# Performance work log

Measured on AMD Instinct MI355X. Metric: run time of the kernel, lower is better.

The kernel has to match this reference:

```python
import jax, jax.numpy as jnp
import numpy as np
import math

HIDDEN = 2048
N_HEADS = 16
N_KV_HEADS = 4
HEAD_DIM = HIDDEN // N_HEADS  # 128
MAX_POS = 4096
ROPE_THETA = 10000.0
B, S = 2, 2048


def _rope_tables():
    freqs = 1.0 / (ROPE_THETA ** (np.arange(0, HEAD_DIM, 2, dtype=np.float32) / HEAD_DIM))
    t = np.arange(MAX_POS, dtype=np.float32)
    f = np.outer(t, freqs)                      # [MAX_POS, HEAD_DIM/2]
    emb = np.concatenate([f, f], axis=-1)       # [MAX_POS, HEAD_DIM]
    return jnp.asarray(np.cos(emb)), jnp.asarray(np.sin(emb))


def setup_inputs() -> dict:
    key = jax.random.key(0)
    ks = jax.random.split(key, 8)
    kv_dim = N_KV_HEADS * HEAD_DIM
    cos, sin = _rope_tables()
    return {
        "hidden_states": jax.random.normal(ks[0], (B, S, HIDDEN), jnp.float32),
        "attention_mask": jnp.zeros((B, S), jnp.float32),
        "position_ids": jnp.arange(S, dtype=jnp.int64 if jax.config.read('jax_enable_x64') else jnp.int32)[None, :],
        "q_w": jax.random.normal(ks[1], (HIDDEN, HIDDEN), jnp.float32) * 0.02,
        "q_b": jnp.zeros((HIDDEN,), jnp.float32),
        "k_w": jax.random.normal(ks[2], (kv_dim, HIDDEN), jnp.float32) * 0.02,
        "k_b": jnp.zeros((kv_dim,), jnp.float32),
        "v_w": jax.random.normal(ks[3], (kv_dim, HIDDEN), jnp.float32) * 0.02,
        "v_b": jnp.zeros((kv_dim,), jnp.float32),
        "o_w": jax.random.normal(ks[4], (HIDDEN, HIDDEN), jnp.float32) * 0.02,
        "cos": cos,
        "sin": sin,
    }


def _rotate_half(x):
    x1, x2 = jnp.split(x, 2, axis=-1)
    return jnp.concatenate([-x2, x1], axis=-1)


def reference(hidden_states, attention_mask, position_ids, q_w, q_b, k_w, k_b,
              v_w, v_b, o_w, cos, sin):
    b, s, _ = hidden_states.shape
    # projections (torch Linear: y = x @ W.T + b)
    q = jnp.einsum('bsi,oi->bso', hidden_states, q_w) + q_b
    k = jnp.einsum('bsi,oi->bso', hidden_states, k_w) + k_b
    v = jnp.einsum('bsi,oi->bso', hidden_states, v_w) + v_b
    q = q.reshape(b, s, N_HEADS, HEAD_DIM).transpose(0, 2, 1, 3)      # [b,h,s,d]
    k = k.reshape(b, s, N_KV_HEADS, HEAD_DIM).transpose(0, 2, 1, 3)   # [b,kv,s,d]
    v = v.reshape(b, s, N_KV_HEADS, HEAD_DIM).transpose(0, 2, 1, 3)
    # RoPE: gather per-position cos/sin, broadcast over heads
    c = cos[position_ids][:, None, :, :]   # [1,1,s,d]
    sn = sin[position_ids][:, None, :, :]
    q = q * c + _rotate_half(q) * sn
    k = k * c + _rotate_half(k) * sn
    # GQA: repeat-interleave kv heads to match query heads
    g = N_HEADS // N_KV_HEADS
    k = jnp.repeat(k, g, axis=1)
    v = jnp.repeat(v, g, axis=1)
    scores = jnp.einsum('bhqd,bhkd->bhqk', q, k) / math.sqrt(HEAD_DIM)
    scores = scores + attention_mask[:, None, None, :]
    attn = jax.nn.softmax(scores.astype(jnp.float32), axis=-1).astype(q.dtype)
    out = jnp.einsum('bhqk,bhkd->bhqd', attn, v)
    out = out.transpose(0, 2, 1, 3).reshape(b, s, HIDDEN)
    return jnp.einsum('bsi,oi->bso', out, o_w)
```

## Files before the change

### kernel.cpp

```cpp
#include <hip/hip_runtime.h>

#define HIDDEN 2048
#define NH 16
#define NKV 4
#define HD 128
#define Bb 2
#define Ss 2048
#define TOK 4096
#define KVD 512
#define LOG2E 1.4426950408889634f
#define QSCALE (0.08838834764831845f * 1.4426950408889634f)
#define DEFER 11.54f

typedef short short8 __attribute__((ext_vector_type(8)));
typedef float f32x4 __attribute__((ext_vector_type(4)));
typedef float f32x16 __attribute__((ext_vector_type(16)));
typedef unsigned int uint4v __attribute__((ext_vector_type(4)));

#define AS1 __attribute__((address_space(1)))
#define AS3 __attribute__((address_space(3)))

#define BARRIER() asm volatile("s_barrier" ::: "memory")
#define WAITV8()  asm volatile("s_waitcnt vmcnt(8)" ::: "memory")
#define WAITV0()  asm volatile("s_waitcnt vmcnt(0)" ::: "memory")

__device__ __forceinline__ float exp2fast(float x){ return __builtin_amdgcn_exp2f(x); }

__device__ __forceinline__ float bf2f(unsigned short u){
  union { unsigned int i; float f; } x; x.i = ((unsigned int)u) << 16; return x.f;
}
__device__ __forceinline__ unsigned short f2bf(float f){
  union { float f; unsigned int i; } x; x.f = f;
  unsigned int r = x.i + 0x7FFFu + ((x.i >> 16) & 1u);
  return (unsigned short)(r >> 16);
}
__device__ __forceinline__ unsigned int cvtpk(float a, float b){
  unsigned int r;
  asm("v_cvt_pk_bf16_f32 %0, %1, %2" : "=v"(r) : "v"(a), "v"(b));
  return r;
}
__device__ __forceinline__ void gld_lds16(const void* g, void* l){
  __builtin_amdgcn_global_load_lds((const AS1 void*)g, (AS3 void*)l, 16, 0, 0);
}

#define R0 2097152
#define R1 3145728
#define R2 3407872
#define R3 3670016
#define R4 4718592
__global__ void cvt_all(const float* __restrict__ s0, const float* __restrict__ s1,
                        const float* __restrict__ s2, const float* __restrict__ s3,
                        const float* __restrict__ s4, unsigned short* __restrict__ dst){
  int i = blockIdx.x * 256 + threadIdx.x;
  const float* src; int off;
  if      (i < R0){ src = s0; off = 0;  }
  else if (i < R1){ src = s1; off = R0; }
  else if (i < R2){ src = s2; off = R1; }
  else if (i < R3){ src = s3; off = R2; }
  else            { src = s4; off = R3; }
  float4 v = reinterpret_cast<const float4*>(src)[i - off];
  ushort4 o;
  o.x = f2bf(v.x); o.y = f2bf(v.y); o.z = f2bf(v.z); o.w = f2bf(v.w);
  reinterpret_cast<ushort4*>(dst)[i] = o;
}

__global__ __launch_bounds__(256, 2) void gemm_nt(
    const unsigned short* __restrict__ A,
    const unsigned short* __restrict__ Bw,
    const float* __restrict__ qb,
    const float* __restrict__ kb,
    const float* __restrict__ vb,
    unsigned short* __restrict__ CbQ,
    unsigned short* __restrict__ CbK,
    unsigned short* __restrict__ vT,
    float* __restrict__ Cf,
    int M, int N, int K, int ldc)
{
  __shared__ unsigned short lds[2][2][128*64];
  const int tid  = threadIdx.x;
  const int lane = tid & 63;
  const int w  = tid >> 6;
  const int wr = w >> 1, wc = w & 1;

  const int nwg  = gridDim.x * gridDim.y;
  const int orig = blockIdx.y * gridDim.x + blockIdx.x;
  const int swz  = (orig & 7) * (nwg >> 3) + (orig >> 3);
  const int row0 = (swz & 31) * 128;
  const int col0 = (swz >> 5) * 128;

  const int fr  = lane & 15;
  const int g16 = lane >> 4;
  const int l8  = lane >> 3;
  const int slot = lane & 7;

  const f32x4 vzero = {0.f, 0.f, 0.f, 0.f};
  f32x4 acc[4][4];
#pragma unroll
  for (int m = 0; m < 4; m++)
#pragma unroll
    for (int n = 0; n < 4; n++) acc[m][n] = vzero;

  auto STAGE = [&](int buf, int kt){
#pragma unroll
    for (int i = 0; i < 4; i++){
      int r = w*32 + i*8 + l8;
      gld_lds16(A  + (size_t)(row0 + r)*K + kt*64 + ((slot ^ (r & 7)) << 3),
                &lds[buf][0][w*2048 + i*512 + lane*8]);
    }
#pragma unroll
    for (int i = 0; i < 4; i++){
      int r = w*32 + i*8 + l8;
      gld_lds16(Bw + (size_t)(col0 + r)*K + kt*64 + ((slot ^ (r & 7)) << 3),
                &lds[buf][1][w*2048 + i*512 + lane*8]);
    }
  };

  const int NT = K >> 6;
  STAGE(0, 0);
  STAGE(1, 1);
  WAITV8();
  BARRIER();

  for (int kt = 0; kt < NT; kt++){
    const int cur = kt & 1;
    const unsigned short* Al = &lds[cur][0][0];
    const unsigned short* Bl = &lds[cur][1][0];
#pragma unroll
    for (int ks = 0; ks < 2; ks++){
      short8 af[4], bf[4];
#pragma unroll
      for (int m = 0; m < 4; m++){
        int r = wr*64 + m*16 + fr;
        af[m] = *(const short8*)&Al[r*64 + (((ks*4 + g16) ^ (r & 7)) << 3)];
      }
#pragma unroll
      for (int n = 0; n < 4; n++){
        int r = wc*64 + n*16 + fr;
        bf[n] = *(const short8*)&Bl[r*64 + (((ks*4 + g16) ^ (r & 7)) << 3)];
      }
      __builtin_amdgcn_s_setprio(1);
#pragma unroll
      for (int m = 0; m < 4; m++)
#pragma unroll
        for (int n = 0; n < 4; n++)
          acc[m][n] = __builtin_amdgcn_mfma_f32_16x16x32_bf16(af[m], bf[n], acc[m][n], 0, 0, 0);
      __builtin_amdgcn_s_setprio(0);
    }
    if (kt == NT - 1) break;
    BARRIER();
    if (kt + 2 < NT){
      STAGE(cur, kt + 2);
      WAITV8();
    } else {
      WAITV0();
    }
    BARRIER();
  }

  const int rr = g16 * 4;
#pragma unroll
  for (int n = 0; n < 4; n++){
    int col = col0 + wc*64 + n*16 + fr;
    float bv = 0.f;
    if (qb) bv = (col < 2048) ? qb[col] : (col < 2560 ? kb[col - 2048] : vb[col - 2560]);
    if (Cf){
#pragma unroll
      for (int m = 0; m < 4; m++){
        int row = row0 + wr*64 + m*16 + rr;
#pragma unroll
        for (int r = 0; r < 4; r++)
          Cf[(size_t)(row + r) * ldc + col] = acc[m][n][r] + bv;
      }
    } else if (col < 2048){
#pragma unroll
      for (int m = 0; m < 4; m++){
        int row = row0 + wr*64 + m*16 + rr;
#pragma unroll
        for (int r = 0; r < 4; r++)
          CbQ[(size_t)(row + r) * 2048 + col] = f2bf(acc[m][n][r] + bv);
      }
    } else if (col < 2560){
      int ck = col - 2048;
#pragma unroll
      for (int m = 0; m < 4; m++){
        int row = row0 + wr*64 + m*16 + rr;
#pragma unroll
        for (int r = 0; r < 4; r++)
          CbK[(size_t)(row + r) * 512 + ck] = f2bf(acc[m][n][r] + bv);
      }
    } else {
      int cv = col - 2560;
#pragma unroll
      for (int m = 0; m < 4; m++){
        int row = row0 + wr*64 + m*16 + rr;
        ushort4 pk;
        pk.x = f2bf(acc[m][n][0] + bv); pk.y = f2bf(acc[m][n][1] + bv);
        pk.z = f2bf(acc[m][n][2] + bv); pk.w = f2bf(acc[m][n][3] + bv);
        *reinterpret_cast<ushort4*>(&vT[(size_t)cv * TOK + row]) = pk;
      }
    }
  }
}

__global__ void rope_kernel(unsigned short* __restrict__ q, unsigned short* __restrict__ k,
                            const int* __restrict__ pos,
                            const float* __restrict__ cosT, const float* __restrict__ sinT)
{
  int idx = blockIdx.x * blockDim.x + threadIdx.x;
  const int qN = TOK * NH * 64;
  if (idx < qN){
    int d  = idx & 63;
    int hh = (idx >> 6) & (NH - 1);
    int t  = idx >> 10;
    int p  = pos[t & (Ss - 1)];
    float c = cosT[p * HD + d], s = sinT[p * HD + d];
    unsigned short* base = q + (size_t)t * HIDDEN + hh * HD;
    float lo = bf2f(base[d]), hi = bf2f(base[d + 64]);
    base[d]      = f2bf((lo * c - hi * s) * QSCALE);
    base[d + 64] = f2bf((hi * c + lo * s) * QSCALE);
  } else {
    int j  = idx - qN;
    int d  = j & 63;
    int hh = (j >> 6) & (NKV - 1);
    int t  = j >> 8;
    int p  = pos[t & (Ss - 1)];
    float c = cosT[p * HD + d], s = sinT[p * HD + d];
    unsigned short* base = k + (size_t)t * KVD + hh * HD;
    float lo = bf2f(base[d]), hi = bf2f(base[d + 64]);
    base[d]      = f2bf(lo * c - hi * s);
    base[d + 64] = f2bf(hi * c + lo * s);
  }
}

__global__ __launch_bounds__(256, 2) void attn_kernel(
    const unsigned short* __restrict__ Q,
    const unsigned short* __restrict__ Kb,
    const unsigned short* __restrict__ Vt,
    const float* __restrict__ mask,
    unsigned short* __restrict__ O)
{
  __shared__ unsigned short Klds[64*128];
  __shared__ unsigned short Vlds[128*64];

  const int tid = threadIdx.x, lane = tid & 63, wid = tid >> 6;
  const int qt = blockIdx.x, kvh = blockIdx.y, b = blockIdx.z;
  const int head = kvh*4 + wid;
  const int q0 = lane & 31;
  const int h  = lane >> 5;
  const int tokQ = b*Ss + qt*32;

  short8 qf[8];
#pragma unroll
  for (int ds = 0; ds < 8; ds++)
    qf[ds] = *(const short8*)(Q + (size_t)(tokQ + q0)*HIDDEN + head*HD + ds*16 + h*8);

  f32x16 oacc[4];
#pragma unroll
  for (int dblk = 0; dblk < 4; dblk++)
#pragma unroll
    for (int r = 0; r < 16; r++) oacc[dblk][r] = 0.f;
  float mrow = -1e30f, lrow = 0.f;

  const float* maskrow = mask + b*Ss;

  const int kk0 = tid >> 4;
  const int kd  = tid & 15;
  const int dv0 = tid >> 3;
  const int vk  = tid & 7;

  const size_t kgbase = (size_t)(b*Ss)*KVD + (size_t)kvh*HD;
  const size_t vgbase = (size_t)(kvh*HD)*TOK + (size_t)(b*Ss);

  short8 kpre[4], vpre[4];
  auto LOADREG = [&](int tok){
#pragma unroll
    for (int i = 0; i < 4; i++){
      kpre[i] = *(const short8*)(Kb + kgbase + (size_t)(tok + kk0 + i*16)*KVD + kd*8);
      vpre[i] = *(const short8*)(Vt + vgbase + (size_t)(dv0 + i*32)*TOK + tok + vk*8);
    }
  };
  auto WRITELDS = [&](){
#pragma unroll
    for (int i = 0; i < 4; i++){
      int kk = kk0 + i*16;
      *(short8*)&Klds[kk*128 + ((kd*8) ^ ((kk & 7) << 3))] = kpre[i];
      int dv = dv0 + i*32;
      *(short8*)&Vlds[dv*64 + ((vk*8) ^ ((dv & 7) << 3))] = vpre[i];
    }
  };

  const int NT = Ss/64;
  LOADREG(0);

  for (int kt = 0; kt < NT; kt++){
    if (kt) __syncthreads();
    WRITELDS();
    __syncthreads();
    if (kt + 1 < NT) LOADREG((kt + 1)*64);

    f32x16 st0, st1;
#pragma unroll
    for (int r = 0; r < 16; r++){ st0[r] = 0.f; st1[r] = 0.f; }
    __builtin_amdgcn_s_setprio(1);
#pragma unroll
    for (int ds = 0; ds < 8; ds++){
      short8 kf0 = *(const short8*)&Klds[(q0     )*128 + ((ds*16 + h*8) ^ ((q0 & 7) << 3))];
      short8 kf1 = *(const short8*)&Klds[(32 + q0)*128 + ((ds*16 + h*8) ^ ((q0 & 7) << 3))];
      st0 = __builtin_amdgcn_mfma_f32_32x32x16_bf16(kf0, qf[ds], st0, 0, 0, 0);
      st1 = __builtin_amdgcn_mfma_f32_32x32x16_bf16(kf1, qf[ds], st1, 0, 0, 0);
    }
    __builtin_amdgcn_s_setprio(0);

    float p[32];
#pragma unroll
    for (int g2 = 0; g2 < 4; g2++){
      f32x4 m0 = *(const f32x4*)(maskrow + kt*64      + g2*8 + h*4);
      f32x4 m1 = *(const f32x4*)(maskrow + kt*64 + 32 + g2*8 + h*4);
#pragma unroll
      for (int r = 0; r < 4; r++){
        p[g2*4 + r]      = st0[g2*4 + r] + m0[r] * LOG2E;
        p[16 + g2*4 + r] = st1[g2*4 + r] + m1[r] * LOG2E;
      }
    }

    float vmax = p[0];
#pragma unroll
    for (int i = 1; i < 32; i++) vmax = fmaxf(vmax, p[i]);
    vmax = fmaxf(vmax, __shfl_xor(vmax, 32));
    if (__any(vmax > mrow + DEFER)){
      float mnew = fmaxf(mrow, vmax);
      float sc = exp2fast(mrow - mnew);
      mrow = mnew; lrow *= sc;
#pragma unroll
      for (int reg = 0; reg < 16; reg++){
        float scr = __shfl(sc, (reg & 3) + 8*(reg >> 2) + 4*h);
#pragma unroll
        for (int dblk = 0; dblk < 4; dblk++) oacc[dblk][reg] *= scr;
      }
    }
    float rs = 0.f;
#pragma unroll
    for (int i = 0; i < 32; i++){ p[i] = exp2fast(p[i] - mrow); rs += p[i]; }
    rs += __shfl_xor(rs, 32);
    lrow += rs;

    unsigned int pk[8][2];
#pragma unroll
    for (int G = 0; G < 8; G++){
      pk[G][0] = cvtpk(p[G*4 + 0], p[G*4 + 1]);
      pk[G][1] = cvtpk(p[G*4 + 2], p[G*4 + 3]);
    }
    short8 pa[4];
#pragma unroll
    for (int ks = 0; ks < 4; ks++){
      const int ia = 4*(ks >> 1) + 2*(ks & 1);
      unsigned int A0 = pk[ia][0],   A1 = pk[ia][1];
      unsigned int B0 = pk[ia+1][0], B1 = pk[ia+1][1];
      unsigned int s0 = h ? A0 : B0, s1 = h ? A1 : B1;
      unsigned int r0 = (unsigned int)__shfl_xor((int)s0, 32);
      unsigned int r1 = (unsigned int)__shfl_xor((int)s1, 32);
      uint4v wv = { h ? r0 : A0, h ? r1 : A1, h ? B0 : r0, h ? B1 : r1 };
      pa[ks] = __builtin_bit_cast(short8, wv);
    }

    __builtin_amdgcn_s_setprio(1);
#pragma unroll
    for (int dblk = 0; dblk < 4; dblk++){
#pragma unroll
      for (int ks = 0; ks < 4; ks++){
        short8 vb = *(const short8*)&Vlds[(dblk*32 + q0)*64 + ((ks*16 + h*8) ^ ((q0 & 7) << 3))];
        oacc[dblk] = __builtin_amdgcn_mfma_f32_32x32x16_bf16(pa[ks], vb, oacc[dblk], 0, 0, 0);
      }
    }
    __builtin_amdgcn_s_setprio(0);
  }

  float inv = 1.0f / lrow;
#pragma unroll
  for (int reg = 0; reg < 16; reg++){
    const int crow = (reg & 3) + 8*(reg >> 2) + 4*h;
    float invr = __shfl(inv, crow);
    int row = tokQ + crow;
#pragma unroll
    for (int dblk = 0; dblk < 4; dblk++)
      O[(size_t)row*HIDDEN + head*HD + dblk*32 + q0] = f2bf(oacc[dblk][reg] * invr);
  }
}

extern "C" void kernel_launch(void* const* d_in, const int* in_sizes, int n_in,
                              void* d_out, int out_size, void* d_ws, size_t ws_size,
                              hipStream_t stream)
{
  (void)in_sizes; (void)n_in; (void)out_size; (void)ws_size;
  const float* hs   = (const float*)d_in[0];
  const float* mask = (const float*)d_in[1];
  const int*   pos  = (const int*)d_in[2];
  const float* qw   = (const float*)d_in[3];
  const float* qb   = (const float*)d_in[4];
  const float* kw   = (const float*)d_in[5];
  const float* kb   = (const float*)d_in[6];
  const float* vw   = (const float*)d_in[7];
  const float* vb   = (const float*)d_in[8];
  const float* ow   = (const float*)d_in[9];
  const float* cosT = (const float*)d_in[10];
  const float* sinT = (const float*)d_in[11];
  float* out = (float*)d_out;

  unsigned short* ws  = (unsigned short*)d_ws;
  unsigned short* hsB = ws;
  unsigned short* qwB = hsB + (size_t)TOK * HIDDEN;
  unsigned short* kwB = qwB + (size_t)HIDDEN * HIDDEN;
  unsigned short* vwB = kwB + (size_t)KVD * HIDDEN;
  unsigned short* owB = vwB + (size_t)KVD * HIDDEN;
  unsigned short* qB  = owB + (size_t)HIDDEN * HIDDEN;
  unsigned short* kB  = qB  + (size_t)TOK * HIDDEN;
  unsigned short* vTB = kB  + (size_t)TOK * KVD;
  unsigned short* aoB = vTB + (size_t)KVD * TOK;
  (void)vwB;

  cvt_all<<<R4 / 256, 256, 0, stream>>>(hs, qw, kw, vw, ow, ws);

  gemm_nt<<<dim3(TOK/128, 3072/128), 256, 0, stream>>>(
      hsB, qwB, qb, kb, vb, qB, kB, vTB, nullptr, TOK, 3072, HIDDEN, 0);

  {
    int total = TOK * NH * 64 + TOK * NKV * 64;
    rope_kernel<<<total / 256, 256, 0, stream>>>(qB, kB, pos, cosT, sinT);
  }

  attn_kernel<<<dim3(Ss/32, NKV, Bb), 256, 0, stream>>>(qB, kB, vTB, mask, aoB);

  gemm_nt<<<dim3(TOK/128, HIDDEN/128), 256, 0, stream>>>(
      aoB, owB, nullptr, nullptr, nullptr, nullptr, nullptr, nullptr, out, TOK, HIDDEN, HIDDEN, HIDDEN);
}
```

Before: 229.5 us.

## Split attention over two KV halves with a log-sum-exp combine kernel

The attention kernel now splits each query tile's key range into two halves across an extra grid dimension, doubling the number of workgroups. Each half writes unnormalized bf16 partial outputs plus its running max and sum, and a new combine kernel merges the two halves. Scratch space from the converted hidden states and Q weights is reused for the second partial output and the statistics. The GEMM's workgroup swizzle is also removed in favour of plain block indexing. The split adds an extra pass over the attention output and an extra bf16 rounding of the partials.

```diff
diff --git a/kernel.cpp b/kernel.cpp
--- a/kernel.cpp
+++ b/kernel.cpp
@@ -81,12 +81,8 @@
   const int lane = tid & 63;
   const int w  = tid >> 6;
   const int wr = w >> 1, wc = w & 1;
-
-  const int nwg  = gridDim.x * gridDim.y;
-  const int orig = blockIdx.y * gridDim.x + blockIdx.x;
-  const int swz  = (orig & 7) * (nwg >> 3) + (orig >> 3);
-  const int row0 = (swz & 31) * 128;
-  const int col0 = (swz >> 5) * 128;
+  const int row0 = blockIdx.x * 128;
+  const int col0 = blockIdx.y * 128;
 
   const int fr  = lane & 15;
   const int g16 = lane >> 4;
@@ -237,13 +233,16 @@
     const unsigned short* __restrict__ Kb,
     const unsigned short* __restrict__ Vt,
     const float* __restrict__ mask,
-    unsigned short* __restrict__ O)
+    unsigned short* __restrict__ O0,
+    unsigned short* __restrict__ O1,
+    float* __restrict__ ml)
 {
   __shared__ unsigned short Klds[64*128];
   __shared__ unsigned short Vlds[128*64];
 
   const int tid = threadIdx.x, lane = tid & 63, wid = tid >> 6;
-  const int qt = blockIdx.x, kvh = blockIdx.y, b = blockIdx.z;
+  const int qt = blockIdx.x, kvh = blockIdx.y;
+  const int b = blockIdx.z >> 1, half = blockIdx.z & 1;
   const int head = kvh*4 + wid;
   const int q0 = lane & 31;
   const int h  = lane >> 5;
@@ -289,14 +288,14 @@
     }
   };
 
-  const int NT = Ss/64;
-  LOADREG(0);
-
-  for (int kt = 0; kt < NT; kt++){
-    if (kt) __syncthreads();
+  const int ktBeg = half * 16, ktEnd = ktBeg + 16;
+  LOADREG(ktBeg * 64);
+
+  for (int kt = ktBeg; kt < ktEnd; kt++){
+    if (kt != ktBeg) __syncthreads();
     WRITELDS();
     __syncthreads();
-    if (kt + 1 < NT) LOADREG((kt + 1)*64);
+    if (kt + 1 < ktEnd) LOADREG((kt + 1)*64);
 
     f32x16 st0, st1;
 #pragma unroll
@@ -375,16 +374,44 @@
     __builtin_amdgcn_s_setprio(0);
   }
 
-  float inv = 1.0f / lrow;
+  unsigned short* Od = half ? O1 : O0;
 #pragma unroll
   for (int reg = 0; reg < 16; reg++){
     const int crow = (reg & 3) + 8*(reg >> 2) + 4*h;
-    float invr = __shfl(inv, crow);
     int row = tokQ + crow;
 #pragma unroll
     for (int dblk = 0; dblk < 4; dblk++)
-      O[(size_t)row*HIDDEN + head*HD + dblk*32 + q0] = f2bf(oacc[dblk][reg] * invr);
-  }
+      Od[(size_t)row*HIDDEN + head*HD + dblk*32 + q0] = f2bf(oacc[dblk][reg]);
+  }
+  if (h == 0){
+    float* mlp = ml + ((size_t)(half*TOK + tokQ + q0) * NH + head) * 2;
+    mlp[0] = mrow; mlp[1] = lrow;
+  }
+}
+
+__global__ void combine_kernel(unsigned short* __restrict__ O0,
+                               const unsigned short* __restrict__ O1,
+                               const float* __restrict__ ml)
+{
+  int e = blockIdx.x * 256 + threadIdx.x;
+  int row = e >> 8;
+  int head = (e & 255) >> 4;
+  const float* a = ml + ((size_t)row * NH + head) * 2;
+  const float* c = ml + ((size_t)(TOK + row) * NH + head) * 2;
+  float m0 = a[0], l0 = a[1], m1 = c[0], l1 = c[1];
+  float M = fmaxf(m0, m1);
+  float c0 = exp2fast(m0 - M), c1 = exp2fast(m1 - M);
+  float inv = 1.f / (c0 * l0 + c1 * l1);
+  size_t off = (size_t)e * 8;
+  short8 v0 = *(const short8*)&O0[off];
+  short8 v1 = *(const short8*)&O1[off];
+  unsigned short outv[8];
+#pragma unroll
+  for (int j = 0; j < 8; j++){
+    float v = (bf2f((unsigned short)v0[j]) * c0 + bf2f((unsigned short)v1[j]) * c1) * inv;
+    outv[j] = f2bf(v);
+  }
+  *(short8*)&O0[off] = *(const short8*)outv;
 }
 
 extern "C" void kernel_launch(void* const* d_in, const int* in_sizes, int n_in,
@@ -416,6 +443,8 @@
   unsigned short* kB  = qB  + (size_t)TOK * HIDDEN;
   unsigned short* vTB = kB  + (size_t)TOK * KVD;
   unsigned short* aoB = vTB + (size_t)KVD * TOK;
+  unsigned short* O1B = hsB;
+  float*          mlB = (float*)qwB;
   (void)vwB;
 
   cvt_all<<<R4 / 256, 256, 0, stream>>>(hs, qw, kw, vw, ow, ws);
@@ -428,7 +457,9 @@
     rope_kernel<<<total / 256, 256, 0, stream>>>(qB, kB, pos, cosT, sinT);
   }
 
-  attn_kernel<<<dim3(Ss/32, NKV, Bb), 256, 0, stream>>>(qB, kB, vTB, mask, aoB);
+  attn_kernel<<<dim3(Ss/32, NKV, Bb*2), 256, 0, stream>>>(qB, kB, vTB, mask, aoB, O1B, mlB);
+
+  combine_kernel<<<(TOK*HIDDEN/8)/256, 256, 0, stream>>>(aoB, O1B, mlB);
 
   gemm_nt<<<dim3(TOK/128, HIDDEN/128), 256, 0, stream>>>(
       aoB, owB, nullptr, nullptr, nullptr, nullptr, nullptr, nullptr, out, TOK, HIDDEN, HIDDEN, HIDDEN);
```

Measured after the change: 224.8 us. 2.0% less time.

## Load attention K/V tiles directly to LDS and drop GEMM tile swizzle

Applied to the files above, without the earlier changes.

Attention K/V staging now issues global-to-LDS direct loads with a pre-swizzled source address, replacing the register prefetch plus LDS write path. This frees registers and removes the ds_write step. In exchange it loses the next-tile prefetch overlap, since each load now happens right before the barrier. The GEMM also drops its workgroup swizzle in favour of plain blockIdx tile mapping, which may hurt L2 locality.

```diff
diff --git a/kernel.cpp b/kernel.cpp
--- a/kernel.cpp
+++ b/kernel.cpp
@@ -81,12 +81,8 @@
   const int lane = tid & 63;
   const int w  = tid >> 6;
   const int wr = w >> 1, wc = w & 1;
-
-  const int nwg  = gridDim.x * gridDim.y;
-  const int orig = blockIdx.y * gridDim.x + blockIdx.x;
-  const int swz  = (orig & 7) * (nwg >> 3) + (orig >> 3);
-  const int row0 = (swz & 31) * 128;
-  const int col0 = (swz >> 5) * 128;
+  const int row0 = blockIdx.x * 128;
+  const int col0 = blockIdx.y * 128;
 
   const int fr  = lane & 15;
   const int g16 = lane >> 4;
@@ -263,40 +259,26 @@
 
   const float* maskrow = mask + b*Ss;
 
-  const int kk0 = tid >> 4;
-  const int kd  = tid & 15;
-  const int dv0 = tid >> 3;
-  const int vk  = tid & 7;
+  const int krow_l = lane >> 4, kslot = lane & 15;
+  const int vrow_l = lane >> 3, vslot = lane & 7;
 
   const size_t kgbase = (size_t)(b*Ss)*KVD + (size_t)kvh*HD;
   const size_t vgbase = (size_t)(kvh*HD)*TOK + (size_t)(b*Ss);
 
-  short8 kpre[4], vpre[4];
-  auto LOADREG = [&](int tok){
-#pragma unroll
-    for (int i = 0; i < 4; i++){
-      kpre[i] = *(const short8*)(Kb + kgbase + (size_t)(tok + kk0 + i*16)*KVD + kd*8);
-      vpre[i] = *(const short8*)(Vt + vgbase + (size_t)(dv0 + i*32)*TOK + tok + vk*8);
-    }
-  };
-  auto WRITELDS = [&](){
-#pragma unroll
-    for (int i = 0; i < 4; i++){
-      int kk = kk0 + i*16;
-      *(short8*)&Klds[kk*128 + ((kd*8) ^ ((kk & 7) << 3))] = kpre[i];
-      int dv = dv0 + i*32;
-      *(short8*)&Vlds[dv*64 + ((vk*8) ^ ((dv & 7) << 3))] = vpre[i];
-    }
-  };
-
   const int NT = Ss/64;
-  LOADREG(0);
-
   for (int kt = 0; kt < NT; kt++){
     if (kt) __syncthreads();
-    WRITELDS();
+    const int tok = kt*64;
+#pragma unroll
+    for (int i = 0; i < 4; i++){
+      int kr = wid*16 + i*4 + krow_l;
+      gld_lds16(Kb + kgbase + (size_t)(tok + kr)*KVD + ((kslot ^ (kr & 7)) << 3),
+                &Klds[(wid*16 + i*4)*128]);
+      int vr = wid*32 + i*8 + vrow_l;
+      gld_lds16(Vt + vgbase + (size_t)vr*TOK + tok + ((vslot ^ (vr & 7)) << 3),
+                &Vlds[(wid*32 + i*8)*64]);
+    }
     __syncthreads();
-    if (kt + 1 < NT) LOADREG((kt + 1)*64);
 
     f32x16 st0, st1;
 #pragma unroll
```

New measurement: 216.9 us (median of 2 runs). -5.5%, faster.
